# Optimization experiments

Hardware: AMD Instinct MI355X
Metric: run time of the kernel (lower is better)

The kernel has to match this reference:

```python
import jax, jax.numpy as jnp
import numpy as np
import math

EMBED_DIM = 256
NUM_HEADS = 8
HEAD_DIM = EMBED_DIM // NUM_HEADS
SEQ = 512
BSZ = 2


def setup_inputs() -> dict:
    key = jax.random.key(0)
    ks = jax.random.split(key, 9)
    def xavier(k, shape):
        fan_in, fan_out = shape[1], shape[0]
        bound = math.sqrt(6.0 / (fan_in + fan_out))
        return jax.random.uniform(k, shape, jnp.float32, -bound, bound)
    return {
        "query": jax.random.normal(ks[0], (SEQ, BSZ, EMBED_DIM), jnp.float32),
        "key": jax.random.normal(ks[1], (SEQ, BSZ, EMBED_DIM), jnp.float32),
        "value": jax.random.normal(ks[2], (SEQ, BSZ, EMBED_DIM), jnp.float32),
        "rel_pos_embedding": jax.random.normal(ks[3], (BSZ, SEQ, SEQ, EMBED_DIM), jnp.float32),
        "attn_mask": jax.random.normal(ks[4], (SEQ, SEQ), jnp.float32),
        "in_proj_weight": xavier(ks[5], (3 * EMBED_DIM, EMBED_DIM)),
        "in_proj_bias": jnp.zeros((3 * EMBED_DIM,), jnp.float32),
        "out_proj_weight": xavier(ks[6], (EMBED_DIM, EMBED_DIM)),
        "out_proj_bias": jnp.zeros((EMBED_DIM,), jnp.float32),
    }


def reference(query, key, value, rel_pos_embedding, attn_mask,
              in_proj_weight, in_proj_bias, out_proj_weight, out_proj_bias):
    L, B, E = query.shape
    H, D = NUM_HEADS, HEAD_DIM
    # NOTE: original module projects ONLY the query and chunks into q,k,v
    qkv = query @ in_proj_weight.T + in_proj_bias          # (L,B,3E)
    q, k, v = jnp.split(qkv, 3, axis=-1)                    # each (L,B,E)
    # (L,B,E) -> (B*H, L, D)
    def to_heads(t):
        return jnp.swapaxes(t.reshape(L, B * H, D), 0, 1)
    q, k, v = to_heads(q), to_heads(k), to_heads(v)
    scores = jnp.einsum('nld,nmd->nlm', q, k) / math.sqrt(D)  # (B*H,L,L)
    # relative position bias: einsum over UNSCALED q
    q4 = q.reshape(B, H, L, D)
    rel = rel_pos_embedding.reshape(B, L, L, H, D)
    rel_bias = jnp.einsum('bhld,blmhd->bhlm', q4, rel)        # (B,H,L,L)
    scores = scores.reshape(B, H, L, L) + rel_bias
    # additive 2D attn_mask broadcast over batch and heads
    scores = scores + attn_mask[None, None, :, :]
    scores = scores.reshape(B * H, L, L)
    attn = jax.nn.softmax(scores, axis=-1)                    # (B*H,L,L)
    out = jnp.einsum('nlm,nmd->nld', attn, v)                 # (B*H,L,D)
    out = jnp.swapaxes(out, 0, 1).reshape(L, B, E)            # (L,B,E)
    out = out @ out_proj_weight.T + out_proj_bias
    return out, attn
```

## Files before the change

### kernel.cpp

```cpp
#include <hip/hip_runtime.h>
#include <math.h>

#define L_SEQ 512
#define BSZ 2
#define NH 8
#define HD 32
#define E 256
#define SCALE 0.17677669529663687f

__global__ void inproj_kernel(const float* __restrict__ query,
                              const float* __restrict__ W,
                              const float* __restrict__ bias,
                              float* __restrict__ qh,
                              float* __restrict__ kh,
                              float* __restrict__ vh) {
    int r0 = blockIdx.x * 4;
    int t = threadIdx.x;
    __shared__ float xs[4][E];
#pragma unroll
    for (int r = 0; r < 4; ++r) xs[r][t] = query[(size_t)(r0 + r) * E + t];
    __syncthreads();

    int c  = t & 7;
    int cg = t >> 3;
    float* outs[3] = {qh, kh, vh};

#pragma unroll
    for (int p = 0; p < 3; ++p) {
#pragma unroll
        for (int pass = 0; pass < 8; ++pass) {
            int col = pass * 32 + cg;
            const float4* wp = (const float4*)(W + (size_t)(p * E + col) * E);
            float a0 = 0.f, a1 = 0.f, a2 = 0.f, a3 = 0.f;
#pragma unroll
            for (int kk = 0; kk < 8; ++kk) {
                float4 w  = wp[c + kk * 8];
                float4 x0 = ((const float4*)xs[0])[c + kk * 8];
                float4 x1 = ((const float4*)xs[1])[c + kk * 8];
                float4 x2 = ((const float4*)xs[2])[c + kk * 8];
                float4 x3 = ((const float4*)xs[3])[c + kk * 8];
                a0 += w.x * x0.x + w.y * x0.y + w.z * x0.z + w.w * x0.w;
                a1 += w.x * x1.x + w.y * x1.y + w.z * x1.z + w.w * x1.w;
                a2 += w.x * x2.x + w.y * x2.y + w.z * x2.z + w.w * x2.w;
                a3 += w.x * x3.x + w.y * x3.y + w.z * x3.z + w.w * x3.w;
            }
#pragma unroll
            for (int off = 1; off <= 4; off <<= 1) {
                a0 += __shfl_xor(a0, off);
                a1 += __shfl_xor(a1, off);
                a2 += __shfl_xor(a2, off);
                a3 += __shfl_xor(a3, off);
            }
            if (c == 0) {
                int h = col >> 5, d = col & 31;
                float bb = bias[p * E + col];
                float res[4] = {a0, a1, a2, a3};
#pragma unroll
                for (int r = 0; r < 4; ++r) {
                    int row = r0 + r, l = row >> 1, b = row & 1;
                    outs[p][((size_t)(b * NH + h) * L_SEQ + l) * HD + d] = res[r] + bb;
                }
            }
        }
    }
}

__global__ void attn_kernel(const float* __restrict__ qh,
                            const float* __restrict__ kh,
                            const float* __restrict__ vh,
                            const float* __restrict__ rpe,
                            const float* __restrict__ mask,
                            float* __restrict__ attn_out,
                            float* __restrict__ oh) {
    int bid = blockIdx.x;
    int l = bid & (L_SEQ - 1);
    int n = bid >> 9;
    int b = n >> 3, h = n & 7;
    int t = threadIdx.x;

    __shared__ float qs[HD];
    __shared__ float s_lds[L_SEQ];
    __shared__ float redmax[8];
    __shared__ float redsum[8];
    __shared__ float pl[L_SEQ];
    __shared__ float redv[16][HD];

    if (t < HD) qs[t] = qh[((size_t)n * L_SEQ + l) * HD + t];
    __syncthreads();

    int c    = t & 7;
    int mrow = t >> 3;
    float4 qc = ((const float4*)qs)[c];
    const float* kbase = kh + (size_t)n * L_SEQ * HD;
    const float* rbase = rpe + ((size_t)(b * L_SEQ + l) * L_SEQ) * E + h * HD;

#pragma unroll
    for (int mi = 0; mi < 8; ++mi) {
        int m = mi * 64 + mrow;
        float4 kv = *(const float4*)(kbase + (size_t)m * HD + c * 4);
        float4 rv = *(const float4*)(rbase + (size_t)m * E + c * 4);
        float part = (kv.x * qc.x + kv.y * qc.y + kv.z * qc.z + kv.w * qc.w) * SCALE
                   +  rv.x * qc.x + rv.y * qc.y + rv.z * qc.z + rv.w * qc.w;
        part += __shfl_xor(part, 1);
        part += __shfl_xor(part, 2);
        part += __shfl_xor(part, 4);
        if (c == 0) s_lds[m] = part;
    }
    __syncthreads();

    float s = s_lds[t] + mask[l * L_SEQ + t];
    int lane = t & 63, wid = t >> 6;
    float mx = s;
#pragma unroll
    for (int off = 32; off > 0; off >>= 1) mx = fmaxf(mx, __shfl_xor(mx, off));
    if (lane == 0) redmax[wid] = mx;
    __syncthreads();
    float bmax = redmax[0];
#pragma unroll
    for (int i = 1; i < 8; ++i) bmax = fmaxf(bmax, redmax[i]);

    float p = __expf(s - bmax);
    float sm = p;
#pragma unroll
    for (int off = 32; off > 0; off >>= 1) sm += __shfl_xor(sm, off);
    if (lane == 0) redsum[wid] = sm;
    __syncthreads();
    float bsum = 0.f;
#pragma unroll
    for (int i = 0; i < 8; ++i) bsum += redsum[i];

    float pn = p / bsum;
    attn_out[((size_t)n * L_SEQ + l) * L_SEQ + t] = pn;
    pl[t] = pn;
    __syncthreads();

    int d = t & 31;
    int g = t >> 5;
    float acc = 0.f;
    int m0 = g * 32;
#pragma unroll 8
    for (int j = 0; j < 32; ++j) {
        acc += pl[m0 + j] * vh[((size_t)n * L_SEQ + m0 + j) * HD + d];
    }
    redv[g][d] = acc;
    __syncthreads();
    if (t < HD) {
        float ssum = 0.f;
#pragma unroll
        for (int gg = 0; gg < 16; ++gg) ssum += redv[gg][t];
        oh[((size_t)n * L_SEQ + l) * HD + t] = ssum;
    }
}

__global__ void outproj_kernel(const float* __restrict__ oh,
                               const float* __restrict__ W,
                               const float* __restrict__ bias,
                               float* __restrict__ out) {
    int r0 = blockIdx.x * 4;
    int t = threadIdx.x;
    __shared__ float xs[4][E];
#pragma unroll
    for (int r = 0; r < 4; ++r) {
        int row = r0 + r, l = row >> 1, b = row & 1;
        int h = t >> 5, d = t & 31;
        xs[r][t] = oh[((size_t)(b * NH + h) * L_SEQ + l) * HD + d];
    }
    __syncthreads();

    int c  = t & 7;
    int cg = t >> 3;
#pragma unroll
    for (int pass = 0; pass < 8; ++pass) {
        int col = pass * 32 + cg;
        const float4* wp = (const float4*)(W + (size_t)col * E);
        float a0 = 0.f, a1 = 0.f, a2 = 0.f, a3 = 0.f;
#pragma unroll
        for (int kk = 0; kk < 8; ++kk) {
            float4 w  = wp[c + kk * 8];
            float4 x0 = ((const float4*)xs[0])[c + kk * 8];
            float4 x1 = ((const float4*)xs[1])[c + kk * 8];
            float4 x2 = ((const float4*)xs[2])[c + kk * 8];
            float4 x3 = ((const float4*)xs[3])[c + kk * 8];
            a0 += w.x * x0.x + w.y * x0.y + w.z * x0.z + w.w * x0.w;
            a1 += w.x * x1.x + w.y * x1.y + w.z * x1.z + w.w * x1.w;
            a2 += w.x * x2.x + w.y * x2.y + w.z * x2.z + w.w * x2.w;
            a3 += w.x * x3.x + w.y * x3.y + w.z * x3.z + w.w * x3.w;
        }
#pragma unroll
        for (int off = 1; off <= 4; off <<= 1) {
            a0 += __shfl_xor(a0, off);
            a1 += __shfl_xor(a1, off);
            a2 += __shfl_xor(a2, off);
            a3 += __shfl_xor(a3, off);
        }
        if (c == 0) {
            float bb = bias[col];
            float res[4] = {a0, a1, a2, a3};
#pragma unroll
            for (int r = 0; r < 4; ++r) {
                out[(size_t)(r0 + r) * E + col] = res[r] + bb;
            }
        }
    }
}

extern "C" void kernel_launch(void* const* d_in, const int* in_sizes, int n_in,
                              void* d_out, int out_size, void* d_ws, size_t ws_size,
                              hipStream_t stream) {
    const float* query = (const float*)d_in[0];
    const float* rpe   = (const float*)d_in[3];
    const float* mask  = (const float*)d_in[4];
    const float* Win   = (const float*)d_in[5];
    const float* bin   = (const float*)d_in[6];
    const float* Wout  = (const float*)d_in[7];
    const float* bout  = (const float*)d_in[8];

    float* out  = (float*)d_out;
    float* attn = (float*)d_out + (size_t)L_SEQ * BSZ * E;

    float* qh = (float*)d_ws;
    float* kh = qh + (size_t)BSZ * NH * L_SEQ * HD;
    float* vh = kh + (size_t)BSZ * NH * L_SEQ * HD;
    float* oh = vh + (size_t)BSZ * NH * L_SEQ * HD;

    inproj_kernel<<<(L_SEQ * BSZ) / 4, E, 0, stream>>>(query, Win, bin, qh, kh, vh);
    attn_kernel<<<BSZ * NH * L_SEQ, L_SEQ, 0, stream>>>(qh, kh, vh, rpe, mask, attn, oh);
    outproj_kernel<<<(L_SEQ * BSZ) / 4, E, 0, stream>>>(oh, Wout, bout, out);
}
```

Before: 193.0 us.

## Process all heads per query row so rel-pos rows are read contiguously

The attention kernel now runs one block per (batch, query position) covering all 8 heads, not one block per (head, position). Each wave reads full 1 KB rows of the relative-position embedding and of K, so rel_pos traffic becomes contiguous rather than 128-byte strided slices, and it uses nontemporal loads. Q, K and the attention output move to a (B,L,E) layout to match. Softmax and PV then run per-wave, one head per wave, with only wave-local reductions. The cost is fewer blocks with more serial work per thread, and K rows are re-read across blocks.

```diff
diff --git a/kernel.cpp b/kernel.cpp
--- a/kernel.cpp
+++ b/kernel.cpp
@@ -8,11 +8,14 @@
 #define E 256
 #define SCALE 0.17677669529663687f
 
+typedef float f32x4 __attribute__((ext_vector_type(4)));
+
+
 __global__ void inproj_kernel(const float* __restrict__ query,
                               const float* __restrict__ W,
                               const float* __restrict__ bias,
-                              float* __restrict__ qh,
-                              float* __restrict__ kh,
+                              float* __restrict__ q2,
+                              float* __restrict__ k2,
                               float* __restrict__ vh) {
     int r0 = blockIdx.x * 4;
     int t = threadIdx.x;
@@ -23,7 +26,6 @@
 
     int c  = t & 7;
     int cg = t >> 3;
-    float* outs[3] = {qh, kh, vh};
 
 #pragma unroll
     for (int p = 0; p < 3; ++p) {
@@ -52,107 +54,114 @@
                 a3 += __shfl_xor(a3, off);
             }
             if (c == 0) {
-                int h = col >> 5, d = col & 31;
                 float bb = bias[p * E + col];
                 float res[4] = {a0, a1, a2, a3};
 #pragma unroll
                 for (int r = 0; r < 4; ++r) {
                     int row = r0 + r, l = row >> 1, b = row & 1;
-                    outs[p][((size_t)(b * NH + h) * L_SEQ + l) * HD + d] = res[r] + bb;
+                    float val = res[r] + bb;
+                    if (p == 0) {
+                        q2[((size_t)b * L_SEQ + l) * E + col] = val;
+                    } else if (p == 1) {
+                        k2[((size_t)b * L_SEQ + l) * E + col] = val;
+                    } else {
+                        int h = col >> 5, d = col & 31;
+                        vh[((size_t)(b * NH + h) * L_SEQ + l) * HD + d] = val;
+                    }
                 }
             }
         }
     }
 }
 
-__global__ void attn_kernel(const float* __restrict__ qh,
-                            const float* __restrict__ kh,
+__global__ void attn_kernel(const float* __restrict__ q2,
+                            const float* __restrict__ k2,
                             const float* __restrict__ vh,
                             const float* __restrict__ rpe,
                             const float* __restrict__ mask,
                             float* __restrict__ attn_out,
-                            float* __restrict__ oh) {
+                            float* __restrict__ oh2) {
     int bid = blockIdx.x;
-    int l = bid & (L_SEQ - 1);
-    int n = bid >> 9;
-    int b = n >> 3, h = n & 7;
+    int b = bid >> 9, l = bid & (L_SEQ - 1);
     int t = threadIdx.x;
-
-    __shared__ float qs[HD];
-    __shared__ float s_lds[L_SEQ];
-    __shared__ float redmax[8];
-    __shared__ float redsum[8];
-    __shared__ float pl[L_SEQ];
-    __shared__ float redv[16][HD];
-
-    if (t < HD) qs[t] = qh[((size_t)n * L_SEQ + l) * HD + t];
-    __syncthreads();
-
-    int c    = t & 7;
-    int mrow = t >> 3;
-    float4 qc = ((const float4*)qs)[c];
-    const float* kbase = kh + (size_t)n * L_SEQ * HD;
-    const float* rbase = rpe + ((size_t)(b * L_SEQ + l) * L_SEQ) * E + h * HD;
-
-#pragma unroll
-    for (int mi = 0; mi < 8; ++mi) {
-        int m = mi * 64 + mrow;
-        float4 kv = *(const float4*)(kbase + (size_t)m * HD + c * 4);
-        float4 rv = *(const float4*)(rbase + (size_t)m * E + c * 4);
+    int lane = t & 63, wid = t >> 6;
+
+    __shared__ float qs[E];
+    __shared__ float s_lds[NH][L_SEQ + 1];
+
+    if (t < E) qs[t] = q2[((size_t)b * L_SEQ + l) * E + t];
+    __syncthreads();
+
+    float4 qc = ((const float4*)qs)[lane];
+    int h1 = lane >> 3;
+    const float* kbase = k2 + (size_t)b * L_SEQ * E;
+    const float* rbase = rpe + ((size_t)(b * L_SEQ + l)) * L_SEQ * E;
+
+#pragma unroll 4
+    for (int i = 0; i < 64; ++i) {
+        int m = wid * 64 + i;
+        float4 kv = ((const float4*)(kbase + (size_t)m * E))[lane];
+        f32x4 rv = __builtin_nontemporal_load(((const f32x4*)(rbase + (size_t)m * E)) + lane);
         float part = (kv.x * qc.x + kv.y * qc.y + kv.z * qc.z + kv.w * qc.w) * SCALE
                    +  rv.x * qc.x + rv.y * qc.y + rv.z * qc.z + rv.w * qc.w;
         part += __shfl_xor(part, 1);
         part += __shfl_xor(part, 2);
         part += __shfl_xor(part, 4);
-        if (c == 0) s_lds[m] = part;
-    }
-    __syncthreads();
-
-    float s = s_lds[t] + mask[l * L_SEQ + t];
-    int lane = t & 63, wid = t >> 6;
-    float mx = s;
+        if ((lane & 7) == 0) s_lds[h1][m] = part;
+    }
+    __syncthreads();
+
+    int h = wid;
+    const float* mrow = mask + (size_t)l * L_SEQ;
+    float sv[8];
+    float mx = -1e30f;
+#pragma unroll
+    for (int i = 0; i < 8; ++i) {
+        int m = i * 64 + lane;
+        sv[i] = s_lds[h][m] + mrow[m];
+        mx = fmaxf(mx, sv[i]);
+    }
 #pragma unroll
     for (int off = 32; off > 0; off >>= 1) mx = fmaxf(mx, __shfl_xor(mx, off));
-    if (lane == 0) redmax[wid] = mx;
-    __syncthreads();
-    float bmax = redmax[0];
-#pragma unroll
-    for (int i = 1; i < 8; ++i) bmax = fmaxf(bmax, redmax[i]);
-
-    float p = __expf(s - bmax);
-    float sm = p;
-#pragma unroll
-    for (int off = 32; off > 0; off >>= 1) sm += __shfl_xor(sm, off);
-    if (lane == 0) redsum[wid] = sm;
-    __syncthreads();
-    float bsum = 0.f;
-#pragma unroll
-    for (int i = 0; i < 8; ++i) bsum += redsum[i];
-
-    float pn = p / bsum;
-    attn_out[((size_t)n * L_SEQ + l) * L_SEQ + t] = pn;
-    pl[t] = pn;
-    __syncthreads();
-
-    int d = t & 31;
-    int g = t >> 5;
-    float acc = 0.f;
-    int m0 = g * 32;
-#pragma unroll 8
-    for (int j = 0; j < 32; ++j) {
-        acc += pl[m0 + j] * vh[((size_t)n * L_SEQ + m0 + j) * HD + d];
-    }
-    redv[g][d] = acc;
-    __syncthreads();
-    if (t < HD) {
-        float ssum = 0.f;
-#pragma unroll
-        for (int gg = 0; gg < 16; ++gg) ssum += redv[gg][t];
-        oh[((size_t)n * L_SEQ + l) * HD + t] = ssum;
-    }
-}
-
-__global__ void outproj_kernel(const float* __restrict__ oh,
+    float sum = 0.f;
+#pragma unroll
+    for (int i = 0; i < 8; ++i) { sv[i] = __expf(sv[i] - mx); sum += sv[i]; }
+#pragma unroll
+    for (int off = 32; off > 0; off >>= 1) sum += __shfl_xor(sum, off);
+    float inv = 1.0f / sum;
+
+    float* arow = attn_out + ((size_t)(b * NH + h) * L_SEQ + l) * L_SEQ;
+#pragma unroll
+    for (int i = 0; i < 8; ++i) {
+        int m = i * 64 + lane;
+        float pn = sv[i] * inv;
+        arow[m] = pn;
+        s_lds[h][m] = pn;
+    }
+
+    int dq = lane & 7, mg = lane >> 3;
+    const float4* vbase = (const float4*)(vh + (size_t)(b * NH + h) * L_SEQ * HD);
+    float4 acc = {0.f, 0.f, 0.f, 0.f};
+#pragma unroll 4
+    for (int i = 0; i < 64; ++i) {
+        int m = i * 8 + mg;
+        float4 v4 = vbase[(size_t)m * 8 + dq];
+        float p = s_lds[h][m];
+        acc.x += p * v4.x; acc.y += p * v4.y; acc.z += p * v4.z; acc.w += p * v4.w;
+    }
+#pragma unroll
+    for (int off = 8; off <= 32; off <<= 1) {
+        acc.x += __shfl_xor(acc.x, off);
+        acc.y += __shfl_xor(acc.y, off);
+        acc.z += __shfl_xor(acc.z, off);
+        acc.w += __shfl_xor(acc.w, off);
+    }
+    if (mg == 0) {
+        ((float4*)(oh2 + ((size_t)b * L_SEQ + l) * E))[h * 8 + dq] = acc;
+    }
+}
+
+__global__ void outproj_kernel(const float* __restrict__ oh2,
                                const float* __restrict__ W,
                                const float* __restrict__ bias,
                                float* __restrict__ out) {
@@ -162,8 +171,7 @@
 #pragma unroll
     for (int r = 0; r < 4; ++r) {
         int row = r0 + r, l = row >> 1, b = row & 1;
-        int h = t >> 5, d = t & 31;
-        xs[r][t] = oh[((size_t)(b * NH + h) * L_SEQ + l) * HD + d];
+        xs[r][t] = oh2[((size_t)b * L_SEQ + l) * E + t];
     }
     __syncthreads();
 
@@ -218,12 +226,12 @@
     float* out  = (float*)d_out;
     float* attn = (float*)d_out + (size_t)L_SEQ * BSZ * E;
 
-    float* qh = (float*)d_ws;
-    float* kh = qh + (size_t)BSZ * NH * L_SEQ * HD;
-    float* vh = kh + (size_t)BSZ * NH * L_SEQ * HD;
-    float* oh = vh + (size_t)BSZ * NH * L_SEQ * HD;
-
-    inproj_kernel<<<(L_SEQ * BSZ) / 4, E, 0, stream>>>(query, Win, bin, qh, kh, vh);
-    attn_kernel<<<BSZ * NH * L_SEQ, L_SEQ, 0, stream>>>(qh, kh, vh, rpe, mask, attn, oh);
-    outproj_kernel<<<(L_SEQ * BSZ) / 4, E, 0, stream>>>(oh, Wout, bout, out);
-}
+    float* q2  = (float*)d_ws;
+    float* k2  = q2 + (size_t)BSZ * L_SEQ * E;
+    float* vh  = k2 + (size_t)BSZ * L_SEQ * E;
+    float* oh2 = vh + (size_t)BSZ * NH * L_SEQ * HD;
+
+    inproj_kernel<<<(L_SEQ * BSZ) / 4, E, 0, stream>>>(query, Win, bin, q2, k2, vh);
+    attn_kernel<<<BSZ * L_SEQ, 512, 0, stream>>>(q2, k2, vh, rpe, mask, attn, oh2);
+    outproj_kernel<<<(L_SEQ * BSZ) / 4, E, 0, stream>>>(oh2, Wout, bout, out);
+}
```

Result: faster. 165.1 us (-14.5%).
